# Performance work log

Measured on AMD Instinct MI355X. Metric: run time of the kernel, lower is better.

The kernel has to match this reference:

```python
import jax, jax.numpy as jnp
import numpy as np


def log_g(x):
    # log of g(x) = where(x>=0, x+0.5, sigmoid(x)), computed stably in log space
    return jnp.where(x >= 0, jnp.log(jax.nn.relu(x) + 0.5), -jax.nn.softplus(-x))


def setup_inputs() -> dict:
    key = jax.random.key(0)
    k1, k2 = jax.random.split(key)
    B, S, D = 4, 4096, 1024
    x = jax.random.normal(k1, (B, S, D), dtype=jnp.float32)
    W_hg = jax.random.normal(k2, (2 * D, D), dtype=jnp.float32) * (1.0 / np.sqrt(D))
    return {"x": x, "W_hg": W_hg}


def reference(x, W_hg):
    # x: [B, S, D], W_hg: [2D, D]
    hg = jnp.einsum('bsd,ed->bse', x, W_hg)  # [B, S, 2D]
    hidden, gate = jnp.split(hg, 2, axis=-1)

    log_coeffs = -jax.nn.softplus(gate)       # log(1 - z)
    log_z = -jax.nn.softplus(-gate)            # log(z)
    log_values = log_z + log_g(hidden)

    # Heinsen associative scan in log space along seq axis
    a_star = jnp.cumsum(log_coeffs, axis=1)
    log_h0_plus_b_star = jax.lax.cumlogsumexp(log_values - a_star, axis=1)
    log_h = a_star + log_h0_plus_b_star
    out = jnp.exp(log_h)  # [B, S, D]; to_out is Identity (expansion_factor=1.0)
    return out
```

## Files before the change

kernel.cpp:

```cpp
#include <hip/hip_runtime.h>
#include <stdint.h>

#define B_ 4
#define S_ 4096
#define D_ 1024
#define E_ 2048
#define K_ 1024
#define M_ (B_*S_)
#define NCHAIN 32
#define SENT 0xFFFFFFFFFFFFFFFFull

typedef __bf16 bf16x8 __attribute__((ext_vector_type(8)));
typedef float  f32x4  __attribute__((ext_vector_type(4)));
typedef _Float16 f16x2 __attribute__((ext_vector_type(2)));

__device__ __forceinline__ unsigned short f2bf(float f) {
    union { float f; unsigned int u; } x; x.f = f;
    unsigned int u = x.u;
    return (unsigned short)((u + 0x7fffu + ((u >> 16) & 1u)) >> 16);
}

__device__ __forceinline__ void gload16(const void* g, void* l) {
    __builtin_amdgcn_global_load_lds(
        (const __attribute__((address_space(1))) void*)(uintptr_t)g,
        (__attribute__((address_space(3))) void*)(uintptr_t)l,
        16, 0, 0);
}

__device__ __forceinline__ unsigned int packCV(float hid, float gat) {
    float e  = __expf(gat);
    float c  = __builtin_amdgcn_rcpf(1.f + e);
    float gg = (hid >= 0.f) ? (hid + 0.5f)
                            : __builtin_amdgcn_rcpf(1.f + __expf(-hid));
    float v  = (1.f - c) * gg;
    union { f16x2 h; unsigned int u; } pk;
    pk.h[0] = (_Float16)c; pk.h[1] = (_Float16)v;
    return pk.u;
}

__global__ __launch_bounds__(256)
void cvt_xw(const float* __restrict__ x, unsigned short* __restrict__ xb,
            const float* __restrict__ w, unsigned short* __restrict__ wb,
            unsigned long long* __restrict__ segAgg) {
    const int b = blockIdx.x;
    const int t = threadIdx.x;
    if (b < 2048) {
        const float4* xp = (const float4*)x + (size_t)b * 2048 + t;
        ushort4*      op = (ushort4*)xb + (size_t)b * 2048 + t;
        float4 f[8];
#pragma unroll
        for (int k = 0; k < 8; k++) f[k] = xp[(size_t)k * 256];
#pragma unroll
        for (int k = 0; k < 8; k++) {
            ushort4 o;
            o.x = f2bf(f[k].x); o.y = f2bf(f[k].y);
            o.z = f2bf(f[k].z); o.w = f2bf(f[k].w);
            op[(size_t)k * 256] = o;
        }
    } else if (b < 2304) {
        const int base4 = (b - 2048) * 2048 + t;
        float4 f[8];
        const float* srcs[8];
#pragma unroll
        for (int k = 0; k < 8; k++) {
            int i = (base4 + k * 256) * 4;
            int r = i >> 10;
            int kk = i & 1023;
            int d = r >> 1, g = r & 1;
            srcs[k] = w + (size_t)(g * D_ + d) * K_ + kk;
        }
#pragma unroll
        for (int k = 0; k < 8; k++) f[k] = *(const float4*)srcs[k];
#pragma unroll
        for (int k = 0; k < 8; k++) {
            int i = (base4 + k * 256) * 4;
            ushort4 o;
            o.x = f2bf(f[k].x); o.y = f2bf(f[k].y);
            o.z = f2bf(f[k].z); o.w = f2bf(f[k].w);
            *(ushort4*)(wb + i) = o;
        }
    } else {
        const size_t base = (size_t)(b - 2304) * 2048 + t;
#pragma unroll
        for (int k = 0; k < 8; k++) segAgg[base + (size_t)k * 256] = SENT;
    }
}

#define BM 128
#define BN 128
#define BK 32

__global__ __launch_bounds__(256, 3)
void gemm_fused(const unsigned short* __restrict__ xb,
                const unsigned short* __restrict__ wb,
                unsigned long long* __restrict__ segAgg,
                float* __restrict__ out) {
    __shared__ unsigned short As[BM * BK];
    __shared__ unsigned short Bs[BN * BK];
    __shared__ __align__(16) unsigned int Ep[4][64][36];

    const int ord   = blockIdx.x;
    const int inner = ord & 63;
    const int eB    = inner >> 2;
    const int bat   = inner & 3;
    const int sIx   = ord >> 6;
    const int mB    = bat * NCHAIN + sIx;
    const int mBase = mB * BM;
    const int eBase = eB * BN;

    const int tid  = threadIdx.x;
    const int lane = tid & 63;
    const int w    = tid >> 6;
    const int waveM = (w >> 1) * 64;
    const int waveN = (w & 1) * 64;

    f32x4 acc[4][4] = {};

    const int row0 = tid >> 2, cu = tid & 3;
    const unsigned short* aG0 = xb + (size_t)(mBase + row0) * K_ + cu * 8;
    const unsigned short* aG1 = aG0 + (size_t)64 * K_;
    const unsigned short* bG0 = wb + (size_t)(eBase + row0) * K_ + cu * 8;
    const unsigned short* bG1 = bG0 + (size_t)64 * K_;
    unsigned short* aL0 = As + (size_t)(w * 64) * 8;
    unsigned short* aL1 = As + (size_t)(256 + w * 64) * 8;
    unsigned short* bL0 = Bs + (size_t)(w * 64) * 8;
    unsigned short* bL1 = Bs + (size_t)(256 + w * 64) * 8;

    const int mrow = lane & 15;
    const int kg   = (lane >> 4) * 8;

    for (int k0 = 0; k0 < K_; k0 += BK) {
        __syncthreads();
        gload16(aG0 + k0, aL0);
        gload16(aG1 + k0, aL1);
        gload16(bG0 + k0, bL0);
        gload16(bG1 + k0, bL1);
        __syncthreads();

        bf16x8 af[4], bfr[4];
#pragma unroll
        for (int i = 0; i < 4; i++)
            af[i] = *(const bf16x8*)(As + (size_t)(waveM + i * 16 + mrow) * BK + kg);
#pragma unroll
        for (int j = 0; j < 4; j++)
            bfr[j] = *(const bf16x8*)(Bs + (size_t)(waveN + j * 16 + mrow) * BK + kg);
#pragma unroll
        for (int i = 0; i < 4; i++)
#pragma unroll
            for (int j = 0; j < 4; j++)
                acc[i][j] = __builtin_amdgcn_mfma_f32_16x16x32_bf16(af[i], bfr[j], acc[i][j], 0, 0, 0);
    }

    const int q    = lane >> 4;
    const int odd  = lane & 1;
    const int colL = (lane & 15) >> 1;
    unsigned int* EpW = &Ep[w][0][0];

#pragma unroll
    for (int i = 0; i < 4; i++) {
#pragma unroll
        for (int j = 0; j < 4; j++) {
            float o0 = __shfl_xor(acc[i][j][0], 1, 64);
            float o1 = __shfl_xor(acc[i][j][1], 1, 64);
            float o2 = __shfl_xor(acc[i][j][2], 1, 64);
            float o3 = __shfl_xor(acc[i][j][3], 1, 64);
            float m0 = odd ? acc[i][j][2] : acc[i][j][0];
            float m1 = odd ? acc[i][j][3] : acc[i][j][1];
            float p0 = odd ? o2 : o0;
            float p1 = odd ? o3 : o1;
            float h0 = odd ? p0 : m0, g0 = odd ? m0 : p0;
            float h1 = odd ? p1 : m1, g1 = odd ? m1 : p1;
            int row = i * 16 + q * 4 + odd * 2;
            int col = j * 8 + colL;
            EpW[(row    ) * 36 + col] = packCV(h0, g0);
            EpW[(row + 1) * 36 + col] = packCV(h1, g1);
        }
    }

    __syncthreads();
    float* scratch = (float*)As;
    float* hpre    = scratch + 512;

    const int dl = tid & 63;
    const int qt = tid >> 6;
    const int wq = (qt >> 1) * 2 + (dl >> 5);
    const int rB = (qt & 1) * 32;
    const int cc_ = dl & 31;
    const unsigned int* src = &Ep[wq][rB][cc_];
    {
        float C = 1.f, V = 0.f;
#pragma unroll 8
        for (int rr = 0; rr < 32; rr++) {
            union { unsigned int u; f16x2 h; } uu;
            uu.u = src[rr * 36];
            float cv_c = (float)uu.h[0], cv_v = (float)uu.h[1];
            V = fmaf(cv_c, V, cv_v);
            C *= cv_c;
        }
        scratch[(qt * 64 + dl) * 2 + 0] = C;
        scratch[(qt * 64 + dl) * 2 + 1] = V;
    }
    __syncthreads();

    if (tid < 64) {
        float C0 = scratch[(0 * 64 + tid) * 2], V0 = scratch[(0 * 64 + tid) * 2 + 1];
        float C1 = scratch[(1 * 64 + tid) * 2], V1 = scratch[(1 * 64 + tid) * 2 + 1];
        float C2 = scratch[(2 * 64 + tid) * 2], V2 = scratch[(2 * 64 + tid) * 2 + 1];
        float C3 = scratch[(3 * 64 + tid) * 2], V3 = scratch[(3 * 64 + tid) * 2 + 1];
        float Cb = (C0 * C1) * (C2 * C3);
        float Vb = fmaf(C3, fmaf(C2, fmaf(C1, V0, V1), V2), V3);
        union { unsigned long long u; float f[2]; } pk;
        pk.f[0] = Cb; pk.f[1] = Vb;
        __hip_atomic_store(&segAgg[(size_t)ord * 64 + tid], pk.u,
                           __ATOMIC_RELAXED, __HIP_MEMORY_SCOPE_AGENT);

        float h = 0.f;
        const size_t chanB = (size_t)inner * 64 + tid;
#pragma unroll 1
        for (int t0 = 0; t0 < NCHAIN; t0 += 8) {
            if (t0 >= sIx) break;
            unsigned long long vb[8];
#pragma unroll
            for (int k = 0; k < 8; k++)
                vb[k] = (t0 + k < sIx)
                    ? __hip_atomic_load(&segAgg[(size_t)(t0 + k) * 4096 + chanB],
                                        __ATOMIC_RELAXED, __HIP_MEMORY_SCOPE_AGENT)
                    : 0x3f800000ull;
#pragma unroll
            for (int k = 0; k < 8; k++) {
                if (t0 + k < sIx) {
                    while (vb[k] == SENT)
                        vb[k] = __hip_atomic_load(&segAgg[(size_t)(t0 + k) * 4096 + chanB],
                                                  __ATOMIC_RELAXED, __HIP_MEMORY_SCOPE_AGENT);
                }
            }
#pragma unroll
            for (int k = 0; k < 8; k++) {
                union { unsigned long long u; float f[2]; } qd; qd.u = vb[k];
                h = fmaf(qd.f[0], h, qd.f[1]);
            }
        }
        hpre[tid] = h;
    }
    __syncthreads();

    {
        float h = hpre[dl];
        if (qt > 0) h = fmaf(scratch[(0 * 64 + dl) * 2], h, scratch[(0 * 64 + dl) * 2 + 1]);
        if (qt > 1) h = fmaf(scratch[(1 * 64 + dl) * 2], h, scratch[(1 * 64 + dl) * 2 + 1]);
        if (qt > 2) h = fmaf(scratch[(2 * 64 + dl) * 2], h, scratch[(2 * 64 + dl) * 2 + 1]);
        float* outp = out + (size_t)(mBase + qt * 32) * D_ + (eB * 64 + dl);
#pragma unroll 8
        for (int rr = 0; rr < 32; rr++) {
            union { unsigned int u; f16x2 hh; } uu;
            uu.u = src[rr * 36];
            h = fmaf((float)uu.hh[0], h, (float)uu.hh[1]);
            outp[(size_t)rr * D_] = h;
        }
    }
}

extern "C" void kernel_launch(void* const* d_in, const int* in_sizes, int n_in,
                              void* d_out, int out_size, void* d_ws, size_t ws_size,
                              hipStream_t stream) {
    const float* x = (const float*)d_in[0];
    const float* wmat = (const float*)d_in[1];
    float* out = (float*)d_out;
    char* ws = (char*)d_ws;

    unsigned short* xb = (unsigned short*)(ws);
    unsigned short* wb = (unsigned short*)(ws + (32u << 20));
    unsigned long long* segAgg = (unsigned long long*)(ws + (36u << 20));

    cvt_xw<<<2368, 256, 0, stream>>>(x, xb, wmat, wb, segAgg);
    gemm_fused<<<2048, 256, 0, stream>>>(xb, wb, segAgg, out);
}
```

Baseline: 201.3 us.

## Fuse x fp32-to-bf16 conversion into GEMM A-tile load

```diff
diff --git a/kernel.cpp b/kernel.cpp
--- a/kernel.cpp
+++ b/kernel.cpp
@@ -25,6 +25,18 @@
         (const __attribute__((address_space(1))) void*)(uintptr_t)g,
         (__attribute__((address_space(3))) void*)(uintptr_t)l,
         16, 0, 0);
+}
+
+__device__ __forceinline__ unsigned int cvtpk2(float lo, float hi) {
+    union { __bf16 h[2]; unsigned int u; } r;
+    r.h[0] = (__bf16)lo; r.h[1] = (__bf16)hi;
+    return r.u;
+}
+__device__ __forceinline__ uint4 cvt8(float4 a, float4 b) {
+    uint4 q;
+    q.x = cvtpk2(a.x, a.y); q.y = cvtpk2(a.z, a.w);
+    q.z = cvtpk2(b.x, b.y); q.w = cvtpk2(b.z, b.w);
+    return q;
 }
 
 __device__ __forceinline__ unsigned int packCV(float hid, float gat) {
@@ -39,26 +51,12 @@
 }
 
 __global__ __launch_bounds__(256)
-void cvt_xw(const float* __restrict__ x, unsigned short* __restrict__ xb,
-            const float* __restrict__ w, unsigned short* __restrict__ wb,
-            unsigned long long* __restrict__ segAgg) {
+void wcvt(const float* __restrict__ w, unsigned short* __restrict__ wb,
+          unsigned long long* __restrict__ segAgg) {
     const int b = blockIdx.x;
     const int t = threadIdx.x;
-    if (b < 2048) {
-        const float4* xp = (const float4*)x + (size_t)b * 2048 + t;
-        ushort4*      op = (ushort4*)xb + (size_t)b * 2048 + t;
-        float4 f[8];
-#pragma unroll
-        for (int k = 0; k < 8; k++) f[k] = xp[(size_t)k * 256];
-#pragma unroll
-        for (int k = 0; k < 8; k++) {
-            ushort4 o;
-            o.x = f2bf(f[k].x); o.y = f2bf(f[k].y);
-            o.z = f2bf(f[k].z); o.w = f2bf(f[k].w);
-            op[(size_t)k * 256] = o;
-        }
-    } else if (b < 2304) {
-        const int base4 = (b - 2048) * 2048 + t;
+    if (b < 256) {
+        const int base4 = b * 2048 + t;
         float4 f[8];
         const float* srcs[8];
 #pragma unroll
@@ -80,7 +78,7 @@
             *(ushort4*)(wb + i) = o;
         }
     } else {
-        const size_t base = (size_t)(b - 2304) * 2048 + t;
+        const size_t base = (size_t)(b - 256) * 2048 + t;
 #pragma unroll
         for (int k = 0; k < 8; k++) segAgg[base + (size_t)k * 256] = SENT;
     }
@@ -91,7 +89,7 @@
 #define BK 32
 
 __global__ __launch_bounds__(256, 3)
-void gemm_fused(const unsigned short* __restrict__ xb,
+void gemm_fused(const float* __restrict__ x,
                 const unsigned short* __restrict__ wb,
                 unsigned long long* __restrict__ segAgg,
                 float* __restrict__ out) {
@@ -117,12 +115,10 @@
     f32x4 acc[4][4] = {};
 
     const int row0 = tid >> 2, cu = tid & 3;
-    const unsigned short* aG0 = xb + (size_t)(mBase + row0) * K_ + cu * 8;
-    const unsigned short* aG1 = aG0 + (size_t)64 * K_;
+    const float* aF0 = x + (size_t)(mBase + row0) * K_ + cu * 8;
+    const float* aF1 = aF0 + (size_t)64 * K_;
     const unsigned short* bG0 = wb + (size_t)(eBase + row0) * K_ + cu * 8;
     const unsigned short* bG1 = bG0 + (size_t)64 * K_;
-    unsigned short* aL0 = As + (size_t)(w * 64) * 8;
-    unsigned short* aL1 = As + (size_t)(256 + w * 64) * 8;
     unsigned short* bL0 = Bs + (size_t)(w * 64) * 8;
     unsigned short* bL1 = Bs + (size_t)(256 + w * 64) * 8;
 
@@ -130,11 +126,15 @@
     const int kg   = (lane >> 4) * 8;
 
     for (int k0 = 0; k0 < K_; k0 += BK) {
+        float4 a0 = *(const float4*)(aF0 + k0);
+        float4 a1 = *(const float4*)(aF0 + k0 + 4);
+        float4 a2 = *(const float4*)(aF1 + k0);
+        float4 a3 = *(const float4*)(aF1 + k0 + 4);
         __syncthreads();
-        gload16(aG0 + k0, aL0);
-        gload16(aG1 + k0, aL1);
         gload16(bG0 + k0, bL0);
         gload16(bG1 + k0, bL1);
+        *(uint4*)(As + (size_t)tid * 8)        = cvt8(a0, a1);
+        *(uint4*)(As + 2048 + (size_t)tid * 8) = cvt8(a2, a3);
         __syncthreads();
 
         bf16x8 af[4], bfr[4];
@@ -268,10 +268,9 @@
     float* out = (float*)d_out;
     char* ws = (char*)d_ws;
 
-    unsigned short* xb = (unsigned short*)(ws);
-    unsigned short* wb = (unsigned short*)(ws + (32u << 20));
-    unsigned long long* segAgg = (unsigned long long*)(ws + (36u << 20));
-
-    cvt_xw<<<2368, 256, 0, stream>>>(x, xb, wmat, wb, segAgg);
-    gemm_fused<<<2048, 256, 0, stream>>>(xb, wb, segAgg, out);
-}
+    unsigned short* wb = (unsigned short*)(ws);
+    unsigned long long* segAgg = (unsigned long long*)(ws + (4u << 20));
+
+    wcvt<<<320, 256, 0, stream>>>(wmat, wb, segAgg);
+    gemm_fused<<<2048, 256, 0, stream>>>(x, wb, segAgg, out);
+}
```

After: 239.8 us. 1.19x slower.

## Double-buffer GEMM LDS tiles, alias epilogue buffers, use nontemporal output stores

Applied to the files above, without the earlier changes.

```diff
diff --git a/kernel.cpp b/kernel.cpp
--- a/kernel.cpp
+++ b/kernel.cpp
@@ -13,6 +13,10 @@
 typedef __bf16 bf16x8 __attribute__((ext_vector_type(8)));
 typedef float  f32x4  __attribute__((ext_vector_type(4)));
 typedef _Float16 f16x2 __attribute__((ext_vector_type(2)));
+
+#define BM 128
+#define BN 128
+#define BK 32
 
 __device__ __forceinline__ unsigned short f2bf(float f) {
     union { float f; unsigned int u; } x; x.f = f;
@@ -86,18 +90,36 @@
     }
 }
 
-#define BM 128
-#define BN 128
-#define BK 32
+__device__ __forceinline__ void kstep(const unsigned short* Ab, const unsigned short* Bb,
+                                      int waveM, int waveN, int mrow, int kg,
+                                      f32x4 acc[4][4]) {
+    bf16x8 af[4], bfr[4];
+#pragma unroll
+    for (int i = 0; i < 4; i++)
+        af[i] = *(const bf16x8*)(Ab + (size_t)(waveM + i * 16 + mrow) * BK + kg);
+#pragma unroll
+    for (int j = 0; j < 4; j++)
+        bfr[j] = *(const bf16x8*)(Bb + (size_t)(waveN + j * 16 + mrow) * BK + kg);
+#pragma unroll
+    for (int i = 0; i < 4; i++)
+#pragma unroll
+        for (int j = 0; j < 4; j++)
+            acc[i][j] = __builtin_amdgcn_mfma_f32_16x16x32_bf16(af[i], bfr[j], acc[i][j], 0, 0, 0);
+}
 
 __global__ __launch_bounds__(256, 3)
 void gemm_fused(const unsigned short* __restrict__ xb,
                 const unsigned short* __restrict__ wb,
                 unsigned long long* __restrict__ segAgg,
                 float* __restrict__ out) {
-    __shared__ unsigned short As[BM * BK];
-    __shared__ unsigned short Bs[BN * BK];
-    __shared__ __align__(16) unsigned int Ep[4][64][36];
+    __shared__ __align__(16) char smem[39424];
+    unsigned short* A0 = (unsigned short*)(smem);
+    unsigned short* A1 = (unsigned short*)(smem + 8192);
+    unsigned short* Bc0 = (unsigned short*)(smem + 16384);
+    unsigned short* Bc1 = (unsigned short*)(smem + 24576);
+    unsigned int*   EpBase = (unsigned int*)(smem);
+    float* scratch = (float*)(smem + 36864);
+    float* hpre    = (float*)(smem + 38912);
 
     const int ord   = blockIdx.x;
     const int inner = ord & 63;
@@ -121,40 +143,39 @@
     const unsigned short* aG1 = aG0 + (size_t)64 * K_;
     const unsigned short* bG0 = wb + (size_t)(eBase + row0) * K_ + cu * 8;
     const unsigned short* bG1 = bG0 + (size_t)64 * K_;
-    unsigned short* aL0 = As + (size_t)(w * 64) * 8;
-    unsigned short* aL1 = As + (size_t)(256 + w * 64) * 8;
-    unsigned short* bL0 = Bs + (size_t)(w * 64) * 8;
-    unsigned short* bL1 = Bs + (size_t)(256 + w * 64) * 8;
+    const int woff = w * 512;
 
     const int mrow = lane & 15;
     const int kg   = (lane >> 4) * 8;
 
-    for (int k0 = 0; k0 < K_; k0 += BK) {
+#define STAGE(Ab, Bb, kk) do { \
+        gload16(aG0 + (kk), (Ab) + woff); \
+        gload16(aG1 + (kk), (Ab) + 2048 + woff); \
+        gload16(bG0 + (kk), (Bb) + woff); \
+        gload16(bG1 + (kk), (Bb) + 2048 + woff); \
+    } while (0)
+
+    STAGE(A0, Bc0, 0);
+    __syncthreads();
+
+    for (int k0 = 0; k0 < K_; k0 += 2 * BK) {
+        STAGE(A1, Bc1, k0 + BK);
+        __builtin_amdgcn_sched_barrier(0);
+        kstep(A0, Bc0, waveM, waveN, mrow, kg, acc);
         __syncthreads();
-        gload16(aG0 + k0, aL0);
-        gload16(aG1 + k0, aL1);
-        gload16(bG0 + k0, bL0);
-        gload16(bG1 + k0, bL1);
+        if (k0 + 2 * BK < K_) {
+            STAGE(A0, Bc0, k0 + 2 * BK);
+            __builtin_amdgcn_sched_barrier(0);
+        }
+        kstep(A1, Bc1, waveM, waveN, mrow, kg, acc);
         __syncthreads();
-
-        bf16x8 af[4], bfr[4];
-#pragma unroll
-        for (int i = 0; i < 4; i++)
-            af[i] = *(const bf16x8*)(As + (size_t)(waveM + i * 16 + mrow) * BK + kg);
-#pragma unroll
-        for (int j = 0; j < 4; j++)
-            bfr[j] = *(const bf16x8*)(Bs + (size_t)(waveN + j * 16 + mrow) * BK + kg);
-#pragma unroll
-        for (int i = 0; i < 4; i++)
-#pragma unroll
-            for (int j = 0; j < 4; j++)
-                acc[i][j] = __builtin_amdgcn_mfma_f32_16x16x32_bf16(af[i], bfr[j], acc[i][j], 0, 0, 0);
-    }
+    }
+#undef STAGE
 
     const int q    = lane >> 4;
     const int odd  = lane & 1;
     const int colL = (lane & 15) >> 1;
-    unsigned int* EpW = &Ep[w][0][0];
+    unsigned int* EpW = EpBase + w * (64 * 36);
 
 #pragma unroll
     for (int i = 0; i < 4; i++) {
@@ -178,15 +199,13 @@
     }
 
     __syncthreads();
-    float* scratch = (float*)As;
-    float* hpre    = scratch + 512;
 
     const int dl = tid & 63;
     const int qt = tid >> 6;
     const int wq = (qt >> 1) * 2 + (dl >> 5);
     const int rB = (qt & 1) * 32;
     const int cc_ = dl & 31;
-    const unsigned int* src = &Ep[wq][rB][cc_];
+    const unsigned int* src = EpBase + ((size_t)wq * 64 + rB) * 36 + cc_;
     {
         float C = 1.f, V = 0.f;
 #pragma unroll 8
@@ -255,7 +274,7 @@
             union { unsigned int u; f16x2 hh; } uu;
             uu.u = src[rr * 36];
             h = fmaf((float)uu.hh[0], h, (float)uu.hh[1]);
-            outp[(size_t)rr * D_] = h;
+            __builtin_nontemporal_store(h, outp + (size_t)rr * D_);
         }
     }
 }
```

Result: no change. 203.1 us (+0.9%).
